# Performance work log

Measured on AMD Instinct MI355X. Metric: run time of the kernel, lower is better.

The kernel has to match this reference:

```python
import math
import jax, jax.numpy as jnp
import numpy as np

D = 512; H = 8; DH = 64          # d_model, heads, head dim
AB = 8                            # attention block size (BigBird block)
NG, NW, NR = 2, 5, 3              # global / window / random blocks
K = NG + NW + NR                  # attended blocks per query block
NL = 5                            # layers per (encoder|decoder) stack
MAXSEQ = 1024; BS = 4; NM = 4; LAT = 16; FF = 2048


def setup_inputs() -> dict:
    key = jax.random.key(0)
    ks = jax.random.split(key, 20)
    B = 32
    S_enc = MAXSEQ + 1
    nb_enc = (S_enc + AB - 1) // AB   # 129
    nb_dec = MAXSEQ // AB             # 128
    def n(i, shape, s=0.02):
        return jax.random.normal(ks[i], shape, jnp.float32) * s
    return {
        'x': jax.random.normal(ks[0], (B, MAXSEQ, BS * NM), jnp.float32),
        'eps': jax.random.normal(ks[1], (B, LAT), jnp.float32),
        'emb_in': n(2, (S_enc, D)),
        'emb_out': n(3, (MAXSEQ, D)),
        'W_data': n(4, (BS * NM, D)), 'b_data': jnp.zeros((D,), jnp.float32),
        'Wqkv': n(5, (2 * NL, D, 3 * D)), 'bqkv': jnp.zeros((2 * NL, 3 * D), jnp.float32),
        'Wo': n(6, (2 * NL, D, D)), 'bo': jnp.zeros((2 * NL, D), jnp.float32),
        'ln1_g': jnp.ones((2 * NL, D), jnp.float32), 'ln1_b': jnp.zeros((2 * NL, D), jnp.float32),
        'W1': n(7, (2 * NL, D, FF)), 'b1': jnp.zeros((2 * NL, FF), jnp.float32),
        'W2': n(8, (2 * NL, FF, D)), 'b2': jnp.zeros((2 * NL, D), jnp.float32),
        'ln2_g': jnp.ones((2 * NL, D), jnp.float32), 'ln2_b': jnp.zeros((2 * NL, D), jnp.float32),
        'W_mean': n(9, (D, LAT)), 'b_mean': jnp.zeros((LAT,), jnp.float32),
        'W_lv': n(10, (D, LAT)), 'b_lv': jnp.zeros((LAT,), jnp.float32),
        'W_exp': n(11, (LAT, 2 * MAXSEQ)), 'b_exp': jnp.zeros((2 * MAXSEQ,), jnp.float32),
        'W_conv': n(12, (2, D)), 'b_conv': jnp.zeros((D,), jnp.float32),
        'W_seq': n(13, (D, BS * NM)), 'b_seq': jnp.zeros((BS * NM,), jnp.float32),
        'rand_enc': jax.random.randint(ks[14], (nb_enc, NR), 0, nb_enc, jnp.int32),
        'rand_dec': jax.random.randint(ks[15], (nb_dec, NR), 0, nb_dec, jnp.int32),
    }


def _ln(x, g, b):
    m = jnp.mean(x, -1, keepdims=True)
    v = jnp.var(x, -1, keepdims=True)
    return (x - m) * jax.lax.rsqrt(v + 1e-5) * g + b


def _block_index(nb, rand):
    # per query block: NG global blocks, NW window blocks, NR random blocks
    i = jnp.arange(nb)
    g = jnp.broadcast_to(jnp.arange(NG)[None, :], (nb, NG))
    w = i[:, None] + (jnp.arange(NW) - NW // 2)[None, :]
    w_valid = (w >= 0) & (w < nb)
    idx = jnp.concatenate([g, jnp.clip(w, 0, nb - 1), rand], axis=1)          # [nb, K]
    valid = jnp.concatenate([jnp.ones((nb, NG), bool), w_valid,
                             jnp.ones((nb, NR), bool)], axis=1)               # [nb, K]
    return idx, valid


def _sparse_attn(x, Wqkv, bqkv, Wo, bo, rand):
    # BigBird-style block-sparse self attention (global + window + random blocks)
    B, S, _ = x.shape
    nb = (S + AB - 1) // AB
    Sp = nb * AB
    qkv = jnp.pad(x @ Wqkv + bqkv, ((0, 0), (0, Sp - S), (0, 0)))
    q, k, v = jnp.split(qkv, 3, axis=-1)
    def blk(t):  # [B,Sp,D] -> [B,H,nb,AB,DH]
        return t.reshape(B, nb, AB, H, DH).transpose(0, 3, 1, 2, 4)
    q, k, v = blk(q), blk(k), blk(v)
    idx, bvalid = _block_index(nb, rand)
    kg = k[:, :, idx]                      # [B,H,nb,K,AB,DH]
    vg = v[:, :, idx]
    scores = jnp.einsum('bhnqd,bhnkpd->bhnqkp', q, kg) / math.sqrt(DH)  # [B,H,nb,AB,K,AB]
    tok_valid = (jnp.arange(Sp) < S).reshape(nb, AB)
    kmask = bvalid[:, :, None] & tok_valid[idx]                          # [nb,K,AB]
    scores = jnp.where(kmask[None, None, :, None], scores, -1e9)
    attn = jax.nn.softmax(scores.reshape(B, H, nb, AB, K * AB), axis=-1)
    out = jnp.einsum('bhnqk,bhnkd->bhnqd', attn, vg.reshape(B, H, nb, K * AB, DH))
    out = out.transpose(0, 2, 3, 1, 4).reshape(B, Sp, D)[:, :S]
    return out @ Wo + bo


def _layer(x, i, p, rand):
    (Wqkv, bqkv, Wo, bo, ln1_g, ln1_b, W1, b1, W2, b2, ln2_g, ln2_b) = p
    a = _sparse_attn(x, Wqkv[i], bqkv[i], Wo[i], bo[i], rand)
    x = _ln(x + a, ln1_g[i], ln1_b[i])
    f = jax.nn.relu(x @ W1[i] + b1[i]) @ W2[i] + b2[i]
    return _ln(x + f, ln2_g[i], ln2_b[i])


def _forward(x, eps, emb_in, emb_out, W_data, b_data, Wqkv, bqkv, Wo, bo,
             ln1_g, ln1_b, W1, b1, W2, b2, ln2_g, ln2_b, W_mean, b_mean,
             W_lv, b_lv, W_exp, b_exp, W_conv, b_conv, W_seq, b_seq,
             rand_enc, rand_dec):
    B = x.shape[0]
    p = (Wqkv, bqkv, Wo, bo, ln1_g, ln1_b, W1, b1, W2, b2, ln2_g, ln2_b)
    # ---- encode ----
    h = x @ W_data + b_data                                   # [B,1024,512]
    cls = jnp.zeros((B, 1, D), x.dtype)
    h = jnp.concatenate([cls, h], axis=1) + emb_in            # [B,1025,512]
    for i in range(NL):
        h = _layer(h, i, p, rand_enc)
    pooled = h[:, 0]
    mean = pooled @ W_mean + b_mean
    logvar = pooled @ W_lv + b_lv
    # ---- sample (diag-Gaussian rsample) ----
    z = mean + eps * jnp.exp(0.5 * logvar)
    # ---- decode ----
    seq = (z @ W_exp + b_exp).reshape(B, 2, MAXSEQ)           # [B,2,1024]
    d = jnp.einsum('bcs,cd->bsd', seq, W_conv) + b_conv       # 1x1 conv, -> [B,1024,512]
    d = d + emb_out
    for i in range(NL, 2 * NL):
        d = _layer(d, i, p, rand_dec)
    out = d @ W_seq + b_seq                                   # [B,1024,16] (1x1 conv)
    decoded = out.reshape(B, -1, NM)                          # [B,4096,4]
    elbo = jnp.mean(-0.5 * jnp.sum(1.0 + logvar - mean ** 2 - jnp.exp(logvar), axis=1))
    return decoded, elbo


def reference(x, eps, emb_in, emb_out, W_data, b_data, Wqkv, bqkv, Wo, bo,
              ln1_g, ln1_b, W1, b1, W2, b2, ln2_g, ln2_b, W_mean, b_mean,
              W_lv, b_lv, W_exp, b_exp, W_conv, b_conv, W_seq, b_seq,
              rand_enc, rand_dec):
    return _forward(x, eps, emb_in, emb_out, W_data, b_data, Wqkv, bqkv, Wo, bo,
                    ln1_g, ln1_b, W1, b1, W2, b2, ln2_g, ln2_b, W_mean, b_mean,
                    W_lv, b_lv, W_exp, b_exp, W_conv, b_conv, W_seq, b_seq,
                    rand_enc, rand_dec)
```

## Files before the change

### kernel.cpp

```cpp
#include <hip/hip_runtime.h>

typedef unsigned short u16;
typedef __attribute__((ext_vector_type(8))) short short8;
typedef __attribute__((ext_vector_type(4))) float f32x4;

__device__ __forceinline__ float b2f(u16 h) {
  union { unsigned int u; float f; } v; v.u = ((unsigned int)h) << 16; return v.f;
}
__device__ __forceinline__ u16 f2b(float f) {
  union { float f; unsigned int u; } v; v.f = f;
  return (u16)((v.u + 0x7fffu + ((v.u >> 16) & 1u)) >> 16);
}

__device__ __forceinline__ void gload16(const u16* g, u16* l) {
  __builtin_amdgcn_global_load_lds(
      (const __attribute__((address_space(1))) void*)g,
      (__attribute__((address_space(3))) void*)l, 16, 0, 0);
}

#define SENC 1025
#define SPENC 1032
#define NBE 129
#define SDEC 1024
#define NBD 128
#define BATCH 32
#define MENC (BATCH * SPENC)
#define MDEC (BATCH * SDEC)

__global__ void beacon_k(float* out) { if (threadIdx.x == 0) out[0] = 1000.0f; }

__global__ __launch_bounds__(256) void tr_k(const float* __restrict__ W, u16* __restrict__ WT, int K, int N)
{
  __shared__ float sm[32][33];
  int k0 = blockIdx.x * 32, n0 = blockIdx.y * 32;
  const float* Wz = W + (size_t)blockIdx.z * K * N;
  u16* WTz = WT + (size_t)blockIdx.z * K * N;
  int r = threadIdx.x >> 3, c0 = (threadIdx.x & 7) * 4;
  float4 v = *(const float4*)&Wz[(size_t)(k0 + r) * N + n0 + c0];
  sm[r][c0] = v.x; sm[r][c0 + 1] = v.y; sm[r][c0 + 2] = v.z; sm[r][c0 + 3] = v.w;
  __syncthreads();
  ushort4 u;
  u.x = f2b(sm[c0][r]); u.y = f2b(sm[c0 + 1][r]); u.z = f2b(sm[c0 + 2][r]); u.w = f2b(sm[c0 + 3][r]);
  *(ushort4*)&WTz[(size_t)(n0 + r) * K + k0 + c0] = u;
}

__global__ __launch_bounds__(256) void embed_k(const float* __restrict__ x, const float* __restrict__ Wd,
    const float* __restrict__ bd, const float* __restrict__ emb, float* __restrict__ h, u16* __restrict__ hb)
{
  size_t gid = (size_t)blockIdx.x * 256 + threadIdx.x;
  int dd = (int)(gid & 511);
  size_t rs = gid >> 9;
  int s = (int)(rs % SPENC);
  int b = (int)(rs / SPENC);
  float v;
  if (s == 0) {
    v = emb[dd];
  } else if (s < SENC) {
    float acc = bd[dd];
    const float* xr = x + ((size_t)b * 1024 + (s - 1)) * 16;
    #pragma unroll
    for (int j = 0; j < 16; ++j) acc += xr[j] * Wd[j * 512 + dd];
    v = acc + emb[(size_t)s * 512 + dd];
  } else {
    v = 0.f;
  }
  h[gid] = v;
  hb[gid] = f2b(v);
}

template<typename TC, bool RELU, bool RESID, bool ATOMIC>
__global__ __launch_bounds__(256) void mgemm_k(const u16* __restrict__ A, const u16* __restrict__ WT,
    const float* __restrict__ bias, const float* __restrict__ R, TC* __restrict__ C,
    int M, int N, int Kc, int lda, int ldb)
{
  __shared__ __align__(16) u16 sA[3][128 * 32];
  __shared__ __align__(16) u16 sB[3][128 * 32];
  int t = threadIdx.x;
  int n0 = blockIdx.x * 128, m0 = blockIdx.y * 128;
  int koff = blockIdx.z * Kc;
  int lane = t & 63, wave = t >> 6;
  int wm = (wave >> 1) * 64, wn = (wave & 1) * 64;
  int quad = lane >> 4, l15 = lane & 15;

  int r0 = wave * 32 + (lane >> 2);
  int r1 = r0 + 16;
  int sc = lane & 3;
  int c0 = sc ^ ((r0 >> 1) & 3);
  int c1 = sc ^ ((r1 >> 1) & 3);
  int ra0 = m0 + r0; ra0 = ra0 < M ? ra0 : M - 1;
  int ra1 = m0 + r1; ra1 = ra1 < M ? ra1 : M - 1;
  const u16* gA0 = A + (size_t)ra0 * lda + koff + c0 * 8;
  const u16* gA1 = A + (size_t)ra1 * lda + koff + c1 * 8;
  const u16* gB0 = WT + (size_t)(n0 + r0) * ldb + koff + c0 * 8;
  const u16* gB1 = WT + (size_t)(n0 + r1) * ldb + koff + c1 * 8;
  u16* lA0 = &sA[0][(wave * 128 + lane) * 8];
  u16* lA1 = &sA[0][(wave * 128 + 64 + lane) * 8];
  u16* lB0 = &sB[0][(wave * 128 + lane) * 8];
  u16* lB1 = &sB[0][(wave * 128 + 64 + lane) * 8];

  f32x4 acc[4][4];
  #pragma unroll
  for (int i = 0; i < 4; ++i)
    #pragma unroll
    for (int j = 0; j < 4; ++j) acc[i][j] = (f32x4){0.f, 0.f, 0.f, 0.f};

  const int nt = Kc >> 5;
  gload16(gA0, lA0); gload16(gA1, lA1); gload16(gB0, lB0); gload16(gB1, lB1);
  gload16(gA0 + 32, lA0 + 4096); gload16(gA1 + 32, lA1 + 4096);
  gload16(gB0 + 32, lB0 + 4096); gload16(gB1 + 32, lB1 + 4096);

  int cur = 0;
  for (int tt = 0; tt < nt; ++tt) {
    if (tt < nt - 1) {
      asm volatile("s_waitcnt vmcnt(4)" ::: "memory");
    } else {
      asm volatile("s_waitcnt vmcnt(0)" ::: "memory");
    }
    __builtin_amdgcn_s_barrier();
    if (tt + 2 < nt) {
      int k0 = (tt + 2) << 5;
      int nb = tt + 2; nb -= (nb / 3) * 3;
      int off = nb * 4096;
      gload16(gA0 + k0, lA0 + off);
      gload16(gA1 + k0, lA1 + off);
      gload16(gB0 + k0, lB0 + off);
      gload16(gB1 + k0, lB1 + off);
    }
    short8 af[4], bf[4];
    #pragma unroll
    for (int i = 0; i < 4; ++i) {
      int ra = wm + i * 16 + l15;
      af[i] = *(const short8*)&sA[cur][ra * 32 + (quad ^ ((ra >> 1) & 3)) * 8];
    }
    #pragma unroll
    for (int j = 0; j < 4; ++j) {
      int rb = wn + j * 16 + l15;
      bf[j] = *(const short8*)&sB[cur][rb * 32 + (quad ^ ((rb >> 1) & 3)) * 8];
    }
    #pragma unroll
    for (int i = 0; i < 4; ++i)
      #pragma unroll
      for (int j = 0; j < 4; ++j)
        acc[i][j] = __builtin_amdgcn_mfma_f32_16x16x32_bf16(af[i], bf[j], acc[i][j], 0, 0, 0);
    cur = (cur == 2) ? 0 : cur + 1;
  }

  #pragma unroll
  for (int i = 0; i < 4; ++i) {
    int mBase = m0 + wm + i * 16 + quad * 4;
    #pragma unroll
    for (int r = 0; r < 4; ++r) {
      int m = mBase + r;
      if (m < M) {
        #pragma unroll
        for (int j = 0; j < 4; ++j) {
          int n = n0 + wn + j * 16 + l15;
          if constexpr (ATOMIC) {
            float v = acc[i][j][r];
            if (blockIdx.z == 0) v += bias[n];
            unsafeAtomicAdd(&((float*)C)[(size_t)m * N + n], v);
          } else {
            float v = acc[i][j][r] + bias[n];
            if (RESID) v += R[(size_t)m * N + n];
            if (RELU) v = fmaxf(v, 0.f);
            if constexpr (sizeof(TC) == 2) ((u16*)C)[(size_t)m * N + n] = f2b(v);
            else ((float*)C)[(size_t)m * N + n] = v;
          }
        }
      }
    }
  }
}

__global__ __launch_bounds__(256) void ln_k(float* h, u16* __restrict__ hb,
    const float* __restrict__ g, const float* __restrict__ bb)
{
  __shared__ float rs[256], rq[256];
  float* p = h + (size_t)blockIdx.x * 512;
  u16* pb = hb + (size_t)blockIdx.x * 512;
  int t = threadIdx.x;
  float v0 = p[t], v1 = p[t + 256];
  rs[t] = v0 + v1; rq[t] = v0 * v0 + v1 * v1;
  __syncthreads();
  for (int o = 128; o > 0; o >>= 1) {
    if (t < o) { rs[t] += rs[t + o]; rq[t] += rq[t + o]; }
    __syncthreads();
  }
  float mean = rs[0] * (1.f / 512.f);
  float var = fmaxf(rq[0] * (1.f / 512.f) - mean * mean, 0.f);
  float rinv = rsqrtf(var + 1e-5f);
  float o0 = (v0 - mean) * rinv * g[t] + bb[t];
  float o1 = (v1 - mean) * rinv * g[t + 256] + bb[t + 256];
  p[t] = o0; p[t + 256] = o1;
  pb[t] = f2b(o0); pb[t + 256] = f2b(o1);
}

__global__ __launch_bounds__(64) void attnm_k(const u16* __restrict__ qkv, u16* __restrict__ av,
    const int* __restrict__ rnd, int S, int Sp, int nb)
{
  __shared__ __align__(16) u16 Vt[64 * 104];
  __shared__ __align__(16) u16 Pl[16 * 104];
  __shared__ int sJB[10], sVD[10];
  int t = threadIdx.x;
  int n = blockIdx.x % nb;
  int r1 = blockIdx.x / nb;
  int hh = r1 & 7, b = r1 >> 3;
  const u16* base = qkv + (size_t)b * Sp * 1536;
  int l15 = t & 15, quad = t >> 4;

  if (t < 10) {
    int jb, vd;
    if (t < 2) { jb = t; vd = 1; }
    else if (t < 7) {
      int w = n + t - 4;
      vd = (w >= 0 && w < nb) ? 1 : 0;
      jb = w < 0 ? 0 : (w > nb - 1 ? nb - 1 : w);
    } else { jb = rnd[n * 3 + t - 7]; vd = 1; }
    sJB[t] = jb; sVD[t] = vd;
  }
  {
    f32x4 zz = {0.f, 0.f, 0.f, 0.f};
    *(f32x4*)&Vt[t * 104 + 80] = zz;
    *(f32x4*)&Vt[t * 104 + 88] = zz;
    if (t < 16) {
      *(f32x4*)&Pl[t * 104 + 80] = zz;
      *(f32x4*)&Pl[t * 104 + 88] = zz;
    }
  }
  __syncthreads();

  short8 aq0, aq1;
  {
    const u16* qp = base + (size_t)(n * 8 + (l15 & 7)) * 1536 + hh * 64 + quad * 8;
    aq0 = *(const short8*)qp;
    aq1 = *(const short8*)(qp + 32);
  }

  f32x4 s[5];
  float okm[5];
  #pragma unroll
  for (int tile = 0; tile < 5; ++tile) {
    int kb = tile * 2 + (l15 >> 3);
    int tok = sJB[kb] * 8 + (l15 & 7);
    okm[tile] = (sVD[kb] && tok < S) ? 0.f : -3.0e38f;
    const u16* kp = base + (size_t)tok * 1536 + 512 + hh * 64 + quad * 8;
    short8 k0 = *(const short8*)kp;
    short8 k1 = *(const short8*)(kp + 32);
    f32x4 c = {0.f, 0.f, 0.f, 0.f};
    c = __builtin_amdgcn_mfma_f32_16x16x32_bf16(aq0, k0, c, 0, 0, 0);
    c = __builtin_amdgcn_mfma_f32_16x16x32_bf16(aq1, k1, c, 0, 0, 0);
    s[tile] = c;
  }

  u16 vreg[80];
  #pragma unroll
  for (int vt = 0; vt < 10; ++vt) {
    const u16* vp = base + (size_t)(sJB[vt] * 8) * 1536 + 1024 + hh * 64 + t;
    #pragma unroll
    for (int j = 0; j < 8; ++j) vreg[vt * 8 + j] = vp[(size_t)j * 1536];
  }

  f32x4 mx = {-3.0e38f, -3.0e38f, -3.0e38f, -3.0e38f};
  #pragma unroll
  for (int tile = 0; tile < 5; ++tile) {
    #pragma unroll
    for (int r = 0; r < 4; ++r) {
      float v = s[tile][r] * 0.125f + okm[tile];
      s[tile][r] = v;
      mx[r] = fmaxf(mx[r], v);
    }
  }
  #pragma unroll
  for (int off = 1; off < 16; off <<= 1) {
    #pragma unroll
    for (int r = 0; r < 4; ++r) mx[r] = fmaxf(mx[r], __shfl_xor(mx[r], off));
  }
  f32x4 sm = {0.f, 0.f, 0.f, 0.f};
  #pragma unroll
  for (int tile = 0; tile < 5; ++tile) {
    #pragma unroll
    for (int r = 0; r < 4; ++r) {
      float e = __expf(s[tile][r] - mx[r]);
      s[tile][r] = e;
      sm[r] += e;
    }
  }
  #pragma unroll
  for (int off = 1; off < 16; off <<= 1) {
    #pragma unroll
    for (int r = 0; r < 4; ++r) sm[r] += __shfl_xor(sm[r], off);
  }

  #pragma unroll
  for (int tile = 0; tile < 5; ++tile)
    #pragma unroll
    for (int r = 0; r < 4; ++r)
      Pl[(quad * 4 + r) * 104 + tile * 16 + l15] = f2b(s[tile][r]);

  #pragma unroll
  for (int vt = 0; vt < 10; ++vt) {
    short8 w;
    #pragma unroll
    for (int j = 0; j < 8; ++j) ((u16*)&w)[j] = (short)vreg[vt * 8 + j];
    *(short8*)&Vt[t * 104 + vt * 8] = w;
  }
  __syncthreads();

  f32x4 o[4];
  #pragma unroll
  for (int dn = 0; dn < 4; ++dn) o[dn] = (f32x4){0.f, 0.f, 0.f, 0.f};
  #pragma unroll
  for (int ks = 0; ks < 3; ++ks) {
    short8 ap = *(const short8*)&Pl[l15 * 104 + ks * 32 + quad * 8];
    #pragma unroll
    for (int dn = 0; dn < 4; ++dn) {
      short8 bv = *(const short8*)&Vt[(dn * 16 + l15) * 104 + ks * 32 + quad * 8];
      o[dn] = __builtin_amdgcn_mfma_f32_16x16x32_bf16(ap, bv, o[dn], 0, 0, 0);
    }
  }

  if (quad < 2) {
    #pragma unroll
    for (int r = 0; r < 4; ++r) {
      int qi = quad * 4 + r;
      float inv = 1.f / sm[r];
      u16* op = av + ((size_t)b * Sp + n * 8 + qi) * 512 + hh * 64 + l15;
      #pragma unroll
      for (int dn = 0; dn < 4; ++dn)
        op[dn * 16] = f2b(o[dn][r] * inv);
    }
  }
}

__global__ __launch_bounds__(512) void head_k(const float* __restrict__ h,
    const float* __restrict__ Wm, const float* __restrict__ bm,
    const float* __restrict__ Wlv, const float* __restrict__ blv,
    const float* __restrict__ eps, float* __restrict__ z, float* out_elbo)
{
  __shared__ float red[512];
  int t = threadIdx.x;
  int b = t >> 4, i = t & 15;
  const float* p = h + (size_t)b * SPENC * 512;
  float am = bm[i], al = blv[i];
  for (int c = 0; c < 512; ++c) {
    float pv = p[c];
    am += pv * Wm[c * 16 + i];
    al += pv * Wlv[c * 16 + i];
  }
  z[t] = am + eps[t] * expf(0.5f * al);
  red[t] = -0.5f * (1.f + al - am * am - expf(al));
  __syncthreads();
  for (int o = 256; o > 0; o >>= 1) { if (t < o) red[t] += red[t + o]; __syncthreads(); }
  if (t == 0) out_elbo[0] = red[0] * (1.f / 32.f);
}

__global__ __launch_bounds__(256) void seq_k(const float* __restrict__ z, const float* __restrict__ We,
    const float* __restrict__ be, float* __restrict__ seq)
{
  int gid = blockIdx.x * 256 + threadIdx.x;
  int b = gid >> 11, c = gid & 2047;
  float acc = be[c];
  #pragma unroll
  for (int i = 0; i < 16; ++i) acc += z[b * 16 + i] * We[i * 2048 + c];
  seq[gid] = acc;
}

__global__ __launch_bounds__(256) void decinit_k(const float* __restrict__ seq, const float* __restrict__ Wc,
    const float* __restrict__ bc, const float* __restrict__ emb, float* __restrict__ h, u16* __restrict__ hb)
{
  size_t gid = (size_t)blockIdx.x * 256 + threadIdx.x;
  int dd = (int)(gid & 511);
  size_t rs = gid >> 9;
  int s = (int)(rs & 1023);
  int b = (int)(rs >> 10);
  float v = seq[b * 2048 + s] * Wc[dd] + seq[b * 2048 + 1024 + s] * Wc[512 + dd]
          + bc[dd] + emb[(size_t)s * 512 + dd];
  h[gid] = v;
  hb[gid] = f2b(v);
}

__global__ __launch_bounds__(256) void final_k(const float* __restrict__ h, const float* __restrict__ Ws,
    const float* __restrict__ bs, float* __restrict__ out)
{
  int gid = blockIdx.x * 256 + threadIdx.x;
  int nn = gid & 15;
  int rs = gid >> 4;
  const float* p = h + (size_t)rs * 512;
  float acc = bs[nn];
  for (int c = 0; c < 512; ++c) acc += p[c] * Ws[c * 16 + nn];
  out[gid] = acc;
}

extern "C" void kernel_launch(void* const* d_in, const int* in_sizes, int n_in,
                              void* d_out, int out_size, void* d_ws, size_t ws_size,
                              hipStream_t stream) {
  float* out = (float*)d_out;
  (void)out_size; (void)ws_size;

  static const int EXP_DICT[30] = {
    524288, 512, 524800, 524288, 8192, 512, 7864320, 15360, 2621440, 5120,
    5120, 5120, 10485760, 20480, 10485760, 5120, 5120, 5120, 8192, 16,
    8192, 16, 32768, 2048, 1024, 512, 8192, 16, 387, 384 };
  bool dict_ok = (n_in == 30);
  if (dict_ok) for (int i = 0; i < 30; ++i) if (in_sizes[i] != EXP_DICT[i]) { dict_ok = false; break; }
  if (!dict_ok) { beacon_k<<<1, 64, 0, stream>>>(out); return; }

  const float* x      = (const float*)d_in[0];
  const float* eps    = (const float*)d_in[1];
  const float* emb_in = (const float*)d_in[2];
  const float* emb_out= (const float*)d_in[3];
  const float* W_data = (const float*)d_in[4];
  const float* b_data = (const float*)d_in[5];
  const float* Wqkv   = (const float*)d_in[6];
  const float* bqkv   = (const float*)d_in[7];
  const float* Wo     = (const float*)d_in[8];
  const float* bo     = (const float*)d_in[9];
  const float* ln1g   = (const float*)d_in[10];
  const float* ln1b   = (const float*)d_in[11];
  const float* W1     = (const float*)d_in[12];
  const float* b1     = (const float*)d_in[13];
  const float* W2     = (const float*)d_in[14];
  const float* b2     = (const float*)d_in[15];
  const float* ln2g   = (const float*)d_in[16];
  const float* ln2b   = (const float*)d_in[17];
  const float* Wm     = (const float*)d_in[18];
  const float* bm     = (const float*)d_in[19];
  const float* Wlv    = (const float*)d_in[20];
  const float* blv    = (const float*)d_in[21];
  const float* Wexp   = (const float*)d_in[22];
  const float* bexp   = (const float*)d_in[23];
  const float* Wconv  = (const float*)d_in[24];
  const float* bconv  = (const float*)d_in[25];
  const float* Wseq   = (const float*)d_in[26];
  const float* bseq   = (const float*)d_in[27];
  const int* rand_enc = (const int*)d_in[28];
  const int* rand_dec = (const int*)d_in[29];

  char* ws = (char*)d_ws;
  float* h     = (float*)ws;
  u16*   hb    = (u16*)(ws + 67633152);
  u16*   WTqkv = (u16*)(ws + 101449728);
  u16*   WTo   = (u16*)(ws + 117178368);
  u16*   WT1l  = (u16*)(ws + 122421248);
  u16*   WT2l  = (u16*)(ws + 124518400);
  u16*   qkvb  = (u16*)(ws + 126615552);
  u16*   avb   = (u16*)(ws + 126615552 + 50724864);
  u16*   ffnb  = (u16*)(ws + 126615552);
  float* seqb  = (float*)(ws + 194248704);
  float* z     = (float*)(ws + 194510848);

  tr_k<<<dim3(512 / 32, 1536 / 32, 10), 256, 0, stream>>>(Wqkv, WTqkv, 512, 1536);
  tr_k<<<dim3(512 / 32, 512 / 32, 10), 256, 0, stream>>>(Wo, WTo, 512, 512);

  {
    const int M = MENC;
    embed_k<<<(M * 512) / 256, 256, 0, stream>>>(x, W_data, b_data, emb_in, h, hb);
    for (int i = 0; i < 5; ++i) {
      for (int bc = 0; bc < 2; ++bc) {
        size_t roff = (size_t)bc * 16 * SPENC * 512;
        const int Mc = 16 * SPENC;
        const int ty = 129;
        mgemm_k<u16, false, false, false><<<dim3(1536 / 128, ty, 1), 256, 0, stream>>>(
            hb + roff, WTqkv + (size_t)i * 512 * 1536, bqkv + (size_t)i * 1536, nullptr, qkvb, Mc, 1536, 512, 512, 512);
        attnm_k<<<16 * 8 * NBE, 64, 0, stream>>>(qkvb, avb, rand_enc, SENC, SPENC, NBE);
        mgemm_k<float, false, false, true><<<dim3(512 / 128, ty, 2), 256, 0, stream>>>(
            avb, WTo + (size_t)i * 512 * 512, bo + (size_t)i * 512, nullptr, h + roff, Mc, 512, 256, 512, 512);
      }
      ln_k<<<M, 256, 0, stream>>>(h, hb, ln1g + (size_t)i * 512, ln1b + (size_t)i * 512);
      tr_k<<<dim3(512 / 32, 2048 / 32, 1), 256, 0, stream>>>(W1 + (size_t)i * 512 * 2048, WT1l, 512, 2048);
      tr_k<<<dim3(2048 / 32, 512 / 32, 1), 256, 0, stream>>>(W2 + (size_t)i * 2048 * 512, WT2l, 2048, 512);
      for (int off = 0; off < M; off += 16512) {
        const int Mc = 16512;
        const int ty = 129;
        mgemm_k<u16, true, false, false><<<dim3(2048 / 128, ty, 1), 256, 0, stream>>>(
            hb + (size_t)off * 512, WT1l, b1 + (size_t)i * 2048, nullptr, ffnb, Mc, 2048, 512, 512, 512);
        mgemm_k<float, false, false, true><<<dim3(512 / 128, ty, 2), 256, 0, stream>>>(
            ffnb, WT2l, b2 + (size_t)i * 512, nullptr, h + (size_t)off * 512, Mc, 512, 1024, 2048, 2048);
      }
      ln_k<<<M, 256, 0, stream>>>(h, hb, ln2g + (size_t)i * 512, ln2b + (size_t)i * 512);
    }
  }

  head_k<<<1, 512, 0, stream>>>(h, Wm, bm, Wlv, blv, eps, z, out + 524288);
  seq_k<<<256, 256, 0, stream>>>(z, Wexp, bexp, seqb);
  decinit_k<<<(MDEC * 512) / 256, 256, 0, stream>>>(seqb, Wconv, bconv, emb_out, h, hb);

  {
    const int M = MDEC;
    for (int i = 5; i < 10; ++i) {
      for (int bc = 0; bc < 2; ++bc) {
        size_t roff = (size_t)bc * 16 * SDEC * 512;
        const int Mc = 16 * SDEC;
        const int ty = 128;
        mgemm_k<u16, false, false, false><<<dim3(1536 / 128, ty, 1), 256, 0, stream>>>(
            hb + roff, WTqkv + (size_t)i * 512 * 1536, bqkv + (size_t)i * 1536, nullptr, qkvb, Mc, 1536, 512, 512, 512);
        attnm_k<<<16 * 8 * NBD, 64, 0, stream>>>(qkvb, avb, rand_dec, SDEC, SDEC, NBD);
        mgemm_k<float, false, false, true><<<dim3(512 / 128, ty, 2), 256, 0, stream>>>(
            avb, WTo + (size_t)i * 512 * 512, bo + (size_t)i * 512, nullptr, h + roff, Mc, 512, 256, 512, 512);
      }
      ln_k<<<M, 256, 0, stream>>>(h, hb, ln1g + (size_t)i * 512, ln1b + (size_t)i * 512);
      tr_k<<<dim3(512 / 32, 2048 / 32, 1), 256, 0, stream>>>(W1 + (size_t)i * 512 * 2048, WT1l, 512, 2048);
      tr_k<<<dim3(2048 / 32, 512 / 32, 1), 256, 0, stream>>>(W2 + (size_t)i * 2048 * 512, WT2l, 2048, 512);
      for (int off = 0; off < M; off += 16384) {
        const int Mc = 16384;
        const int ty = 128;
        mgemm_k<u16, true, false, false><<<dim3(2048 / 128, ty, 1), 256, 0, stream>>>(
            hb + (size_t)off * 512, WT1l, b1 + (size_t)i * 2048, nullptr, ffnb, Mc, 2048, 512, 512, 512);
        mgemm_k<float, false, false, true><<<dim3(512 / 128, ty, 2), 256, 0, stream>>>(
            ffnb, WT2l, b2 + (size_t)i * 512, nullptr, h + (size_t)off * 512, Mc, 512, 1024, 2048, 2048);
      }
      ln_k<<<M, 256, 0, stream>>>(h, hb, ln2g + (size_t)i * 512, ln2b + (size_t)i * 512);
    }
  }

  final_k<<<524288 / 256, 256, 0, stream>>>(h, Wseq, bseq, out);
}
```

Baseline: 7.175 ms.

## Widen GEMM tile to 128x256 with 8 waves, double buffering, XCD-aware block swizzle

The bf16 MFMA GEMM now uses 512-thread workgroups computing 128x256 output tiles, which gives more reuse of each A tile per LDS load. The 3-stage async prefetch with manual vmcnt waits is replaced by a 2-stage double buffer synchronised with __syncthreads. A block-index remap groups consecutive tiles onto the same XCD to improve L2 locality. Shallower prefetch may expose more load latency, and the larger block may lower occupancy.

```diff
diff --git a/kernel.cpp b/kernel.cpp
--- a/kernel.cpp
+++ b/kernel.cpp
@@ -69,34 +69,39 @@
 }
 
 template<typename TC, bool RELU, bool RESID, bool ATOMIC>
-__global__ __launch_bounds__(256) void mgemm_k(const u16* __restrict__ A, const u16* __restrict__ WT,
+__global__ __launch_bounds__(512) void mgemm_k(const u16* __restrict__ A, const u16* __restrict__ WT,
     const float* __restrict__ bias, const float* __restrict__ R, TC* __restrict__ C,
     int M, int N, int Kc, int lda, int ldb)
 {
-  __shared__ __align__(16) u16 sA[3][128 * 32];
-  __shared__ __align__(16) u16 sB[3][128 * 32];
+  __shared__ __align__(16) u16 sA[2][128 * 32];
+  __shared__ __align__(16) u16 sB[2][256 * 32];
   int t = threadIdx.x;
-  int n0 = blockIdx.x * 128, m0 = blockIdx.y * 128;
+
+  int gx = gridDim.x;
+  int nwg = gx * gridDim.y;
+  int flat = blockIdx.y * gx + blockIdx.x;
+  int q = nwg >> 3, rr = nwg & 7;
+  int xcd = flat & 7, idx = flat >> 3;
+  int swz = (xcd < rr ? xcd * (q + 1) : rr * (q + 1) + (xcd - rr) * q) + idx;
+  int bx = swz % gx, by = swz / gx;
+
+  int n0 = bx * 256, m0 = by * 128;
   int koff = blockIdx.z * Kc;
   int lane = t & 63, wave = t >> 6;
-  int wm = (wave >> 1) * 64, wn = (wave & 1) * 64;
+  int wm = (wave >> 2) * 64, wn = (wave & 3) * 64;
   int quad = lane >> 4, l15 = lane & 15;
 
-  int r0 = wave * 32 + (lane >> 2);
-  int r1 = r0 + 16;
-  int sc = lane & 3;
-  int c0 = sc ^ ((r0 >> 1) & 3);
-  int c1 = sc ^ ((r1 >> 1) & 3);
-  int ra0 = m0 + r0; ra0 = ra0 < M ? ra0 : M - 1;
-  int ra1 = m0 + r1; ra1 = ra1 < M ? ra1 : M - 1;
-  const u16* gA0 = A + (size_t)ra0 * lda + koff + c0 * 8;
-  const u16* gA1 = A + (size_t)ra1 * lda + koff + c1 * 8;
-  const u16* gB0 = WT + (size_t)(n0 + r0) * ldb + koff + c0 * 8;
-  const u16* gB1 = WT + (size_t)(n0 + r1) * ldb + koff + c1 * 8;
-  u16* lA0 = &sA[0][(wave * 128 + lane) * 8];
-  u16* lA1 = &sA[0][(wave * 128 + 64 + lane) * 8];
-  u16* lB0 = &sB[0][(wave * 128 + lane) * 8];
-  u16* lB1 = &sB[0][(wave * 128 + 64 + lane) * 8];
+  int rA = t >> 2, sc = t & 3;
+  int cA = sc ^ ((rA >> 1) & 3);
+  int raA = m0 + rA; raA = raA < M ? raA : M - 1;
+  const u16* gA  = A  + (size_t)raA * lda + koff + cA * 8;
+  int rB = t >> 2;
+  int cB = sc ^ ((rB >> 1) & 3);
+  const u16* gB0 = WT + (size_t)(n0 + rB) * ldb + koff + cB * 8;
+  const u16* gB1 = WT + (size_t)(n0 + 128 + rB) * ldb + koff + cB * 8;
+  u16* lA  = &sA[0][t * 8];
+  u16* lB0 = &sB[0][t * 8];
+  u16* lB1 = &sB[0][(512 + t) * 8];
 
   f32x4 acc[4][4];
   #pragma unroll
@@ -105,26 +110,15 @@
     for (int j = 0; j < 4; ++j) acc[i][j] = (f32x4){0.f, 0.f, 0.f, 0.f};
 
   const int nt = Kc >> 5;
-  gload16(gA0, lA0); gload16(gA1, lA1); gload16(gB0, lB0); gload16(gB1, lB1);
-  gload16(gA0 + 32, lA0 + 4096); gload16(gA1 + 32, lA1 + 4096);
-  gload16(gB0 + 32, lB0 + 4096); gload16(gB1 + 32, lB1 + 4096);
-
+  gload16(gA, lA); gload16(gB0, lB0); gload16(gB1, lB1);
   int cur = 0;
   for (int tt = 0; tt < nt; ++tt) {
-    if (tt < nt - 1) {
-      asm volatile("s_waitcnt vmcnt(4)" ::: "memory");
-    } else {
-      asm volatile("s_waitcnt vmcnt(0)" ::: "memory");
-    }
-    __builtin_amdgcn_s_barrier();
-    if (tt + 2 < nt) {
-      int k0 = (tt + 2) << 5;
-      int nb = tt + 2; nb -= (nb / 3) * 3;
-      int off = nb * 4096;
-      gload16(gA0 + k0, lA0 + off);
-      gload16(gA1 + k0, lA1 + off);
-      gload16(gB0 + k0, lB0 + off);
-      gload16(gB1 + k0, lB1 + off);
+    __syncthreads();
+    if (tt + 1 < nt) {
+      int k0 = (tt + 1) << 5;
+      gload16(gA + k0, lA + (cur ^ 1) * 4096);
+      gload16(gB0 + k0, lB0 + (cur ^ 1) * 8192);
+      gload16(gB1 + k0, lB1 + (cur ^ 1) * 8192);
     }
     short8 af[4], bf[4];
     #pragma unroll
@@ -142,7 +136,7 @@
       #pragma unroll
       for (int j = 0; j < 4; ++j)
         acc[i][j] = __builtin_amdgcn_mfma_f32_16x16x32_bf16(af[i], bf[j], acc[i][j], 0, 0, 0);
-    cur = (cur == 2) ? 0 : cur + 1;
+    cur ^= 1;
   }
 
   #pragma unroll
@@ -460,10 +454,10 @@
         size_t roff = (size_t)bc * 16 * SPENC * 512;
         const int Mc = 16 * SPENC;
         const int ty = 129;
-        mgemm_k<u16, false, false, false><<<dim3(1536 / 128, ty, 1), 256, 0, stream>>>(
+        mgemm_k<u16, false, false, false><<<dim3(1536 / 256, ty, 1), 512, 0, stream>>>(
             hb + roff, WTqkv + (size_t)i * 512 * 1536, bqkv + (size_t)i * 1536, nullptr, qkvb, Mc, 1536, 512, 512, 512);
         attnm_k<<<16 * 8 * NBE, 64, 0, stream>>>(qkvb, avb, rand_enc, SENC, SPENC, NBE);
-        mgemm_k<float, false, false, true><<<dim3(512 / 128, ty, 2), 256, 0, stream>>>(
+        mgemm_k<float, false, false, true><<<dim3(512 / 256, ty, 2), 512, 0, stream>>>(
             avb, WTo + (size_t)i * 512 * 512, bo + (size_t)i * 512, nullptr, h + roff, Mc, 512, 256, 512, 512);
       }
       ln_k<<<M, 256, 0, stream>>>(h, hb, ln1g + (size_t)i * 512, ln1b + (size_t)i * 512);
@@ -472,9 +466,9 @@
       for (int off = 0; off < M; off += 16512) {
         const int Mc = 16512;
         const int ty = 129;
-        mgemm_k<u16, true, false, false><<<dim3(2048 / 128, ty, 1), 256, 0, stream>>>(
+        mgemm_k<u16, true, false, false><<<dim3(2048 / 256, ty, 1), 512, 0, stream>>>(
             hb + (size_t)off * 512, WT1l, b1 + (size_t)i * 2048, nullptr, ffnb, Mc, 2048, 512, 512, 512);
-        mgemm_k<float, false, false, true><<<dim3(512 / 128, ty, 2), 256, 0, stream>>>(
+        mgemm_k<float, false, false, true><<<dim3(512 / 256, ty, 2), 512, 0, stream>>>(
             ffnb, WT2l, b2 + (size_t)i * 512, nullptr, h + (size_t)off * 512, Mc, 512, 1024, 2048, 2048);
       }
       ln_k<<<M, 256, 0, stream>>>(h, hb, ln2g + (size_t)i * 512, ln2b + (size_t)i * 512);
@@ -492,10 +486,10 @@
         size_t roff = (size_t)bc * 16 * SDEC * 512;
         const int Mc = 16 * SDEC;
         const int ty = 128;
-        mgemm_k<u16, false, false, false><<<dim3(1536 / 128, ty, 1), 256, 0, stream>>>(
+        mgemm_k<u16, false, false, false><<<dim3(1536 / 256, ty, 1), 512, 0, stream>>>(
             hb + roff, WTqkv + (size_t)i * 512 * 1536, bqkv + (size_t)i * 1536, nullptr, qkvb, Mc, 1536, 512, 512, 512);
         attnm_k<<<16 * 8 * NBD, 64, 0, stream>>>(qkvb, avb, rand_dec, SDEC, SDEC, NBD);
-        mgemm_k<float, false, false, true><<<dim3(512 / 128, ty, 2), 256, 0, stream>>>(
+        mgemm_k<float, false, false, true><<<dim3(512 / 256, ty, 2), 512, 0, stream>>>(
             avb, WTo + (size_t)i * 512 * 512, bo + (size_t)i * 512, nullptr, h + roff, Mc, 512, 256, 512, 512);
       }
       ln_k<<<M, 256, 0, stream>>>(h, hb, ln1g + (size_t)i * 512, ln1b + (size_t)i * 512);
@@ -504,9 +498,9 @@
       for (int off = 0; off < M; off += 16384) {
         const int Mc = 16384;
         const int ty = 128;
-        mgemm_k<u16, true, false, false><<<dim3(2048 / 128, ty, 1), 256, 0, stream>>>(
+        mgemm_k<u16, true, false, false><<<dim3(2048 / 256, ty, 1), 512, 0, stream>>>(
             hb + (size_t)off * 512, WT1l, b1 + (size_t)i * 2048, nullptr, ffnb, Mc, 2048, 512, 512, 512);
-        mgemm_k<float, false, false, true><<<dim3(512 / 128, ty, 2), 256, 0, stream>>>(
+        mgemm_k<float, false, false, true><<<dim3(512 / 256, ty, 2), 512, 0, stream>>>(
             ffnb, WT2l, b2 + (size_t)i * 512, nullptr, h + (size_t)off * 512, Mc, 512, 1024, 2048, 2048);
       }
       ln_k<<<M, 256, 0, stream>>>(h, hb, ln2g + (size_t)i * 512, ln2b + (size_t)i * 512);
```

Result: faster. 6.830 ms (-4.8%).
